# Kernel optimization log

Hardware: AMD Instinct MI355X
Metric: run time of the kernel (lower is better)

The kernel has to match this reference:

```python
import math
import jax, jax.numpy as jnp
import numpy as np

B, NQ, NK, DIM, H, HD = 2, 1024, 2048, 1024, 16, 64


def setup_inputs() -> dict:
    key = jax.random.key(0)
    ks = jax.random.split(key, 12)
    s = 1.0 / math.sqrt(DIM)
    return {
        "q": jax.random.normal(ks[0], (B, NQ, DIM), jnp.float32),
        "k": jax.random.normal(ks[1], (B, NK, DIM), jnp.float32),
        "v": jax.random.normal(ks[2], (B, NK, DIM), jnp.float32),
        "distances": jax.random.uniform(ks[3], (B, NQ, NK), jnp.float32),
        "attn_mask": jax.random.bernoulli(ks[4], 0.5, (B, NQ, NK)),
        "key_padding_mask_q": jax.random.bernoulli(ks[5], 0.5, (B, NQ)),
        "key_padding_mask_k": jax.random.bernoulli(ks[6], 0.5, (B, NK)),
        "Wq": jax.random.normal(ks[7], (H * HD, DIM), jnp.float32) * s,
        "Wk": jax.random.normal(ks[8], (H * HD, DIM), jnp.float32) * s,
        "Wv": jax.random.normal(ks[9], (H * HD, DIM), jnp.float32) * s,
        "Wo": jax.random.normal(ks[10], (DIM, H * HD), jnp.float32) * s,
        "gate_alpha": jnp.float32(0.1),
    }


def reference(q, k, v, distances, attn_mask, key_padding_mask_q,
              key_padding_mask_k, Wq, Wk, Wv, Wo, gate_alpha):
    bsz, q_len, _ = q.shape
    k_len = k.shape[1]
    neg = jnp.finfo(q.dtype).min

    # projections -> (B, H, N, HD)
    qp = (q @ Wq.T).reshape(bsz, q_len, H, HD).transpose(0, 2, 1, 3)
    kp = (k @ Wk.T).reshape(bsz, k_len, H, HD).transpose(0, 2, 1, 3)
    vp = (v @ Wv.T).reshape(bsz, k_len, H, HD).transpose(0, 2, 1, 3)

    scores = jnp.einsum('bhqd,bhkd->bhqk', qp, kp) / math.sqrt(HD)
    scores = jnp.where(attn_mask[:, None, :, :], scores, neg)
    scores = jnp.where(key_padding_mask_k[:, None, None, :], scores, neg)

    attn = jax.nn.softmax(scores, axis=-1)  # (B,H,NQ,NK)

    # distance gating: mask, batch-mean normalize, exponential gate
    d = distances * attn_mask.astype(distances.dtype)
    d = d * key_padding_mask_k[:, None, :].astype(d.dtype)
    mean = d.sum(axis=(-1, -2)) / (q_len * k_len + 1e-6)
    mean = jnp.maximum(mean, 1e-6)[:, None, None]
    d = d / mean
    alpha = jax.nn.softplus(gate_alpha)
    gate = jnp.exp(-alpha * d)[:, None, :, :]  # (B,1,NQ,NK)

    w = attn * gate
    w = w / (w.sum(axis=-1, keepdims=True) + 1e-6)

    out = jnp.einsum('bhqk,bhkd->bhqd', w, vp)
    out = out.transpose(0, 2, 1, 3).reshape(bsz, q_len, H * HD)
    out = out * key_padding_mask_q[:, :, None].astype(out.dtype)
    return out @ Wo.T
```

## Files before the change

### kernel.cpp

```cpp
#include <hip/hip_runtime.h>
#include <hip/hip_bf16.h>
#include <cfloat>

#define B_   2
#define NQ_  1024
#define NK_  2048
#define H_   16
#define HD_  64
#define VPAD 2176
#define GPAD 2112

typedef float  floatx4 __attribute__((ext_vector_type(4)));
typedef __bf16 bf16x8  __attribute__((ext_vector_type(8)));
typedef __bf16 bf16x4  __attribute__((ext_vector_type(4)));

static __device__ __forceinline__ floatx4 mfma16(bf16x8 a, bf16x8 b, floatx4 c) {
    return __builtin_amdgcn_mfma_f32_16x16x32_bf16(a, b, c, 0, 0, 0);
}

static __device__ __forceinline__ void gl_lds(const __bf16* g, __bf16* lbase,
                                              int lane) {
#if __has_builtin(__builtin_amdgcn_global_load_lds)
    __builtin_amdgcn_global_load_lds(
        (const __attribute__((address_space(1))) void*)g,
        (__attribute__((address_space(3))) void*)lbase, 16, 0, 0);
#else
    *(bf16x8*)(lbase + lane * 8) = *(const bf16x8*)g;
#endif
}

struct CvtArgs {
    const float* src[7];
    __bf16*      dst[7];
};

__global__ __launch_bounds__(256) void cvt_mean_kernel(
    CvtArgs a, const float* __restrict__ dist, const int* __restrict__ amask,
    const int* __restrict__ kpmk, float* __restrict__ msum,
    __bf16* __restrict__ dmask)
{
    if (blockIdx.x >= 1792) {
        const int mb = blockIdx.x - 1792;
        const int b  = mb >> 9;
        const float* d  = dist  + (size_t)b * NQ_ * NK_;
        const int*   am = amask + (size_t)b * NQ_ * NK_;
        const int*   km = kpmk  + b * NK_;
        __bf16*      dm = dmask + (size_t)b * NQ_ * GPAD;
        const int base = (mb & 511) * 256 + threadIdx.x;
        float s = 0.f;
        #pragma unroll
        for (int j = 0; j < 4; j++) {
            const int i   = base + j * 131072;
            const int idx = i * 4;
            const int kk  = idx & (NK_ - 1);
            const int q   = i >> 9;
            float4 dv = *(const float4*)(d + idx);
            int4   mv = *(const int4*)(am + idx);
            int4   kv = *(const int4*)(km + kk);
            bf16x4 o;
            if (mv.x && kv.x) { s += dv.x; o[0] = (__bf16)dv.x; } else o[0] = (__bf16)3e38f;
            if (mv.y && kv.y) { s += dv.y; o[1] = (__bf16)dv.y; } else o[1] = (__bf16)3e38f;
            if (mv.z && kv.z) { s += dv.z; o[2] = (__bf16)dv.z; } else o[2] = (__bf16)3e38f;
            if (mv.w && kv.w) { s += dv.w; o[3] = (__bf16)dv.w; } else o[3] = (__bf16)3e38f;
            *(bf16x4*)&dm[(size_t)q * GPAD + kk] = o;
        }
        #pragma unroll
        for (int off = 32; off >= 1; off >>= 1) s += __shfl_down(s, off);
        __shared__ float wsum[4];
        if ((threadIdx.x & 63) == 0) wsum[threadIdx.x >> 6] = s;
        __syncthreads();
        if (threadIdx.x == 0)
            atomicAdd(&msum[b], wsum[0] + wsum[1] + wsum[2] + wsum[3]);
        return;
    }
    #pragma unroll
    for (int j = 0; j < 4; j++) {
        size_t r = (size_t)blockIdx.x * 1024 + j * 256 + threadIdx.x;
        int s;
        if (r < 262144)                  { s = 0; }
        else if ((r -= 262144) < 524288) { s = 1; }
        else if ((r -= 524288) < 524288) { s = 2; }
        else { r -= 524288; s = 3 + (int)(r >> 17); r &= 131071; }
        const float* sp = a.src[s] + r * 8;
        float4 f0 = *(const float4*)sp;
        float4 f1 = *(const float4*)(sp + 4);
        bf16x8 o;
        o[0] = (__bf16)f0.x; o[1] = (__bf16)f0.y; o[2] = (__bf16)f0.z; o[3] = (__bf16)f0.w;
        o[4] = (__bf16)f1.x; o[5] = (__bf16)f1.y; o[6] = (__bf16)f1.z; o[7] = (__bf16)f1.w;
        *(bf16x8*)(a.dst[s] + r * 8) = o;
    }
}

template <typename EPI>
static __device__ __forceinline__ void gemm128_core(
    const __bf16* __restrict__ A, const __bf16* __restrict__ Bw,
    int m0, int n0, __bf16* As, __bf16* Bs, EPI epi)
{
    const int t    = threadIdx.x;
    const int w    = t >> 6, lane = t & 63;
    const int lrow = lane & 15, quad = lane >> 4;
    const int lr   = lane >> 2, lc = lane & 3;

    floatx4 acc[4][4];
    #pragma unroll
    for (int mi = 0; mi < 4; mi++)
        #pragma unroll
        for (int ni = 0; ni < 4; ni++) acc[mi][ni] = floatx4{0.f, 0.f, 0.f, 0.f};

    const __bf16* ga = A  + (size_t)(m0 + w * 32 + lr) * 1024 + lc * 8;
    const __bf16* gb = Bw + (size_t)(n0 + w * 32 + lr) * 1024 + lc * 8;

    for (int k0 = 0; k0 < 1024; k0 += 64) {
        __syncthreads();
        #pragma unroll
        for (int h = 0; h < 2; h++) {
            gl_lds(ga + k0 + h * 32,             &As[h * 4096 + (w * 32) * 32],      lane);
            gl_lds(ga + k0 + h * 32 + 16 * 1024, &As[h * 4096 + (w * 32 + 16) * 32], lane);
            gl_lds(gb + k0 + h * 32,             &Bs[h * 4096 + (w * 32) * 32],      lane);
            gl_lds(gb + k0 + h * 32 + 16 * 1024, &Bs[h * 4096 + (w * 32 + 16) * 32], lane);
        }
        __syncthreads();

        #pragma unroll
        for (int h = 0; h < 2; h++) {
            bf16x8 af[4], bfr[4];
            #pragma unroll
            for (int mi = 0; mi < 4; mi++)
                af[mi] = *(const bf16x8*)
                    &As[h * 4096 + ((w & 1) * 64 + mi * 16 + lrow) * 32 + quad * 8];
            #pragma unroll
            for (int ni = 0; ni < 4; ni++)
                bfr[ni] = *(const bf16x8*)
                    &Bs[h * 4096 + ((w >> 1) * 64 + ni * 16 + lrow) * 32 + quad * 8];
            #pragma unroll
            for (int mi = 0; mi < 4; mi++)
                #pragma unroll
                for (int ni = 0; ni < 4; ni++)
                    acc[mi][ni] = mfma16(af[mi], bfr[ni], acc[mi][ni]);
        }
    }

    #pragma unroll
    for (int mi = 0; mi < 4; mi++)
        #pragma unroll
        for (int ni = 0; ni < 4; ni++)
            #pragma unroll
            for (int r = 0; r < 4; r++) {
                const int m = m0 + (w & 1) * 64 + mi * 16 + quad * 4 + r;
                const int n = n0 + (w >> 1) * 64 + ni * 16 + lrow;
                epi(m, n, acc[mi][ni][r]);
            }
}

template <typename EPI>
static __device__ __forceinline__ void gemm32_core(
    const __bf16* __restrict__ A, const __bf16* __restrict__ Bw,
    int m0, int n0, EPI epi)
{
    __shared__ alignas(16) __bf16 As[2][32 * 32];
    __shared__ alignas(16) __bf16 Bs[2][128 * 32];
    const int t    = threadIdx.x;
    const int w    = t >> 6, lane = t & 63;
    const int lrow = lane & 15, quad = lane >> 4;
    const int lr   = lane >> 2, lc = lane & 3;

    floatx4 acc[2][2];
    #pragma unroll
    for (int mi = 0; mi < 2; mi++)
        #pragma unroll
        for (int ni = 0; ni < 2; ni++) acc[mi][ni] = floatx4{0.f, 0.f, 0.f, 0.f};

    const __bf16* ga = A  + (size_t)(m0 + (w & 1) * 16 + lr) * 1024 + lc * 8;
    const __bf16* gb = Bw + (size_t)(n0 + w * 32 + lr) * 1024 + lc * 8;

    for (int k0 = 0; k0 < 1024; k0 += 64) {
        __syncthreads();
        #pragma unroll
        for (int h = 0; h < 2; h++) {
            if (w < 2)
                gl_lds(ga + k0 + h * 32, &As[h][(w * 16) * 32], lane);
            gl_lds(gb + k0 + h * 32,             &Bs[h][(w * 32) * 32],      lane);
            gl_lds(gb + k0 + h * 32 + 16 * 1024, &Bs[h][(w * 32 + 16) * 32], lane);
        }
        __syncthreads();

        #pragma unroll
        for (int h = 0; h < 2; h++) {
            bf16x8 af[2], bfr[2];
            #pragma unroll
            for (int mi = 0; mi < 2; mi++)
                af[mi] = *(const bf16x8*)
                    &As[h][(mi * 16 + lrow) * 32 + quad * 8];
            #pragma unroll
            for (int ni = 0; ni < 2; ni++)
                bfr[ni] = *(const bf16x8*)
                    &Bs[h][(w * 32 + ni * 16 + lrow) * 32 + quad * 8];
            #pragma unroll
            for (int mi = 0; mi < 2; mi++)
                #pragma unroll
                for (int ni = 0; ni < 2; ni++)
                    acc[mi][ni] = mfma16(af[mi], bfr[ni], acc[mi][ni]);
        }
    }

    #pragma unroll
    for (int mi = 0; mi < 2; mi++)
        #pragma unroll
        for (int ni = 0; ni < 2; ni++)
            #pragma unroll
            for (int r = 0; r < 4; r++) {
                const int m = m0 + mi * 16 + quad * 4 + r;
                const int n = n0 + w * 32 + ni * 16 + lrow;
                epi(m, n, acc[mi][ni][r]);
            }
}

__global__ __launch_bounds__(256) void proj_kernel(
    const __bf16* __restrict__ qb, const __bf16* __restrict__ kb,
    const __bf16* __restrict__ vb, const __bf16* __restrict__ wqb,
    const __bf16* __restrict__ wkb, const __bf16* __restrict__ wvb,
    __bf16* __restrict__ qp, __bf16* __restrict__ kp,
    __bf16* __restrict__ vpT)
{
    __shared__ alignas(16) __bf16 As[2 * 128 * 32];
    __shared__ alignas(16) __bf16 Bs[2 * 128 * 32];
    const int z = blockIdx.z;
    if (z == 0) {
        if ((int)blockIdx.x >= 16) return;
        gemm128_core(qb, wqb, blockIdx.x * 128, blockIdx.y * 128, As, Bs,
                     [&](int m, int n, float v) {
            const int b = m >> 10, q = m & 1023;
            const int h = n >> 6,  d = n & 63;
            qp[(((size_t)(b * 16 + h) * NQ_ + q) << 6) + d] = (__bf16)v;
        });
    } else if (z == 1) {
        gemm128_core(kb, wkb, blockIdx.x * 128, blockIdx.y * 128, As, Bs,
                     [&](int m, int n, float v) {
            const int b = m >> 11, key = m & 2047;
            const int h = n >> 6,  d = n & 63;
            kp[(((size_t)(b * 16 + h) * NK_ + key) << 6) + d] = (__bf16)v;
        });
    } else {
        gemm128_core(wvb, vb, blockIdx.y * 128, blockIdx.x * 128, As, Bs,
                     [&](int m, int n, float v) {
            const int h = m >> 6,  d = m & 63;
            const int b = n >> 11, key = n & 2047;
            vpT[((size_t)(b * 16 + h) * HD_ + d) * VPAD + key] = (__bf16)v;
        });
    }
}

__global__ __launch_bounds__(256) void oproj_kernel(
    const __bf16* __restrict__ A, const __bf16* __restrict__ W,
    float* __restrict__ Cout)
{
    const int m0 = blockIdx.x * 32, n0 = blockIdx.y * 128;
    gemm32_core(A, W, m0, n0, [&](int m, int n, float v) {
        Cout[(size_t)m * 1024 + n] = v;
    });
}

__global__ __launch_bounds__(256, 2) void attn_kernel(
    const __bf16* __restrict__ qp, const __bf16* __restrict__ kp,
    const __bf16* __restrict__ vpT, const __bf16* __restrict__ dmask,
    const float* __restrict__ msum, const float* __restrict__ galpha,
    const int* __restrict__ kpmq, __bf16* __restrict__ attnout)
{
    __shared__ __bf16 Ks[64 * 72];
    __shared__ __bf16 Vt[2][64 * 72];
    __shared__ __bf16 Ps[4][2][16 * 72];
    const int t    = threadIdx.x;
    const int w    = t >> 6, lane = t & 63;
    const int lrow = lane & 15, quad = lane >> 4;
    const int qt   = blockIdx.x;
    const int bh   = blockIdx.y;
    const int b    = bh >> 4, h = bh & 15;
    const int q0   = qt * 64 + w * 16;
    const int NT   = NK_ / 64;

    const float mean  = fmaxf(msum[b] / ((float)(NQ_ * NK_) + 1e-6f), 1e-6f);
    const float alpha = log1pf(__expf(galpha[0]));
    const float cg    = -alpha / mean;

    const __bf16* qb = qp + ((size_t)bh * NQ_ + q0 + lrow) * HD_ + quad * 8;
    const bf16x8 qf0 = *(const bf16x8*)qb;
    const bf16x8 qf1 = *(const bf16x8*)(qb + 32);

    const int srow0 = t >> 3,        sc0 = t & 7;
    const int srow1 = 32 + (t >> 3), sc1 = t & 7;
    const int so0 = srow0 * 72 + sc0 * 8;
    const int so1 = srow1 * 72 + sc1 * 8;
    const __bf16* Kg = kp  + (size_t)bh * NK_ * HD_;
    const __bf16* Vg = vpT + (size_t)bh * HD_ * VPAD;
    const __bf16* grow = dmask + ((size_t)b * NQ_ + q0 + lrow) * GPAD;

    float G = 0.f;
    floatx4 O[4];
    #pragma unroll
    for (int nb = 0; nb < 4; nb++) O[nb] = floatx4{0.f, 0.f, 0.f, 0.f};

    bf16x8 kr0, kr1, vr0, vr1;
    bf16x4 gr[4];
    auto loadt = [&](int kb) {
        kr0 = *(const bf16x8*)(Kg + (size_t)(kb + srow0) * HD_ + sc0 * 8);
        kr1 = *(const bf16x8*)(Kg + (size_t)(kb + srow1) * HD_ + sc1 * 8);
        vr0 = *(const bf16x8*)(Vg + (size_t)srow0 * VPAD + kb + sc0 * 8);
        vr1 = *(const bf16x8*)(Vg + (size_t)srow1 * VPAD + kb + sc1 * 8);
        #pragma unroll
        for (int c = 0; c < 4; c++)
            gr[c] = *(const bf16x4*)(grow + kb + c * 16 + quad * 4);
    };
    loadt(0);

    for (int ib = 0; ib < NT; ib++) {
        const int kb  = ib * 64;
        const int cur = ib & 1;

        __syncthreads();
        *(bf16x8*)&Ks[so0]      = kr0;
        *(bf16x8*)&Ks[so1]      = kr1;
        *(bf16x8*)&Vt[cur][so0] = vr0;
        *(bf16x8*)&Vt[cur][so1] = vr1;
        __syncthreads();

        bf16x4 gcur[4];
        #pragma unroll
        for (int c = 0; c < 4; c++) gcur[c] = gr[c];
        if (ib + 1 < NT) loadt(kb + 64);

        floatx4 s4[4];
        #pragma unroll
        for (int c = 0; c < 4; c++) {
            bf16x8 kf0 = *(const bf16x8*)&Ks[(c * 16 + lrow) * 72 + quad * 8];
            bf16x8 kf1 = *(const bf16x8*)&Ks[(c * 16 + lrow) * 72 + 32 + quad * 8];
            floatx4 a = floatx4{0.f, 0.f, 0.f, 0.f};
            a = mfma16(kf0, qf0, a);
            a = mfma16(kf1, qf1, a);
            s4[c] = a;
        }

        if (ib > 0) {
            const int prv = cur ^ 1;
            bf16x8 pf0 = *(const bf16x8*)&Ps[w][prv][lrow * 72 + quad * 8];
            bf16x8 pf1 = *(const bf16x8*)&Ps[w][prv][lrow * 72 + 32 + quad * 8];
            #pragma unroll
            for (int nb = 0; nb < 4; nb++) {
                bf16x8 vf0 = *(const bf16x8*)
                    &Vt[prv][(nb * 16 + lrow) * 72 + quad * 8];
                bf16x8 vf1 = *(const bf16x8*)
                    &Vt[prv][(nb * 16 + lrow) * 72 + 32 + quad * 8];
                O[nb] = mfma16(pf0, vf0, O[nb]);
                O[nb] = mfma16(pf1, vf1, O[nb]);
            }
        }

        #pragma unroll
        for (int c = 0; c < 4; c++) {
            const float e0 = __expf(fmaf(s4[c][0], 0.125f, cg * (float)gcur[c][0]));
            const float e1 = __expf(fmaf(s4[c][1], 0.125f, cg * (float)gcur[c][1]));
            const float e2 = __expf(fmaf(s4[c][2], 0.125f, cg * (float)gcur[c][2]));
            const float e3 = __expf(fmaf(s4[c][3], 0.125f, cg * (float)gcur[c][3]));
            G += (e0 + e1) + (e2 + e3);
            bf16x4 pk;
            pk[0] = (__bf16)e0; pk[1] = (__bf16)e1;
            pk[2] = (__bf16)e2; pk[3] = (__bf16)e3;
            *(bf16x4*)&Ps[w][cur][lrow * 72 + c * 16 + quad * 4] = pk;
        }
    }

    {
        const int prv = (NT - 1) & 1;
        bf16x8 pf0 = *(const bf16x8*)&Ps[w][prv][lrow * 72 + quad * 8];
        bf16x8 pf1 = *(const bf16x8*)&Ps[w][prv][lrow * 72 + 32 + quad * 8];
        #pragma unroll
        for (int nb = 0; nb < 4; nb++) {
            bf16x8 vf0 = *(const bf16x8*)&Vt[prv][(nb * 16 + lrow) * 72 + quad * 8];
            bf16x8 vf1 = *(const bf16x8*)&Vt[prv][(nb * 16 + lrow) * 72 + 32 + quad * 8];
            O[nb] = mfma16(pf0, vf0, O[nb]);
            O[nb] = mfma16(pf1, vf1, O[nb]);
        }
    }

    G += __shfl_xor(G, 16);
    G += __shfl_xor(G, 32);

    #pragma unroll
    for (int r = 0; r < 4; r++) {
        const int q  = q0 + quad * 4 + r;
        const float gq = __shfl(G, quad * 4 + r);
        const float f  = kpmq[b * NQ_ + q] ? 1.f / (gq + 1e-30f) : 0.f;
        #pragma unroll
        for (int nb = 0; nb < 4; nb++) {
            attnout[((size_t)b * NQ_ + q) * 1024 + h * HD_ + nb * 16 + lrow] =
                (__bf16)(O[nb][r] * f);
        }
    }
}

extern "C" void kernel_launch(void* const* d_in, const int* in_sizes, int n_in,
                              void* d_out, int out_size, void* d_ws,
                              size_t ws_size, hipStream_t stream)
{
    const float* q      = (const float*)d_in[0];
    const float* k      = (const float*)d_in[1];
    const float* v      = (const float*)d_in[2];
    const float* dist   = (const float*)d_in[3];
    const int*   amask  = (const int*)d_in[4];
    const int*   kpmq   = (const int*)d_in[5];
    const int*   kpmk   = (const int*)d_in[6];
    const float* Wq     = (const float*)d_in[7];
    const float* Wk     = (const float*)d_in[8];
    const float* Wv     = (const float*)d_in[9];
    const float* Wo     = (const float*)d_in[10];
    const float* galpha = (const float*)d_in[11];

    char* p = (char*)d_ws;
    float*  msum = (float*)p;                 p += 256;
    __bf16* qb   = (__bf16*)p;                p += (size_t)2097152 * 2;
    __bf16* kb   = (__bf16*)p;                p += (size_t)4194304 * 2;
    __bf16* vb   = (__bf16*)p;                p += (size_t)4194304 * 2;
    __bf16* wqb  = (__bf16*)p;                p += (size_t)1048576 * 2;
    __bf16* wkb  = (__bf16*)p;                p += (size_t)1048576 * 2;
    __bf16* wvb  = (__bf16*)p;                p += (size_t)1048576 * 2;
    __bf16* wob  = (__bf16*)p;                p += (size_t)1048576 * 2;
    __bf16* qp   = (__bf16*)p;                p += (size_t)2097152 * 2;
    __bf16* kpb  = (__bf16*)p;                p += (size_t)4194304 * 2;
    __bf16* vpT  = (__bf16*)p;                p += (size_t)32 * 64 * VPAD * 2;
    __bf16* dmask = (__bf16*)p;               p += (size_t)2048 * GPAD * 2;
    __bf16* attnout = (__bf16*)p;             p += (size_t)2097152 * 2;

    CvtArgs ca;
    ca.src[0] = q;  ca.src[1] = k;  ca.src[2] = v;
    ca.src[3] = Wq; ca.src[4] = Wk; ca.src[5] = Wv; ca.src[6] = Wo;
    ca.dst[0] = qb;  ca.dst[1] = kb;  ca.dst[2] = vb;
    ca.dst[3] = wqb; ca.dst[4] = wkb; ca.dst[5] = wvb; ca.dst[6] = wob;

    hipMemsetAsync(msum, 0, 256, stream);
    cvt_mean_kernel<<<2816, 256, 0, stream>>>(ca, dist, amask, kpmk, msum,
                                              dmask);
    proj_kernel<<<dim3(32, 8, 3), 256, 0, stream>>>(qb, kb, vb, wqb, wkb, wvb,
                                                    qp, kpb, vpT);
    attn_kernel<<<dim3(16, 32), 256, 0, stream>>>(qp, kpb, vpT, dmask,
                                                  msum, galpha, kpmq, attnout);
    oproj_kernel<<<dim3(64, 8), 256, 0, stream>>>(attnout, wob, (float*)d_out);
}
```

Before: 246.5 us.

## Split attention over key dimension into two halves with combine kernel

Splits the attention kernel along the key axis into two chunks, which doubles the grid from 512 to 1024 blocks so more CUs stay busy. Each block writes unnormalized fp32 partial outputs and row sums into reused workspace buffers, and a new combine kernel adds the two halves, applies the normalization and the query padding mask, and writes bf16. Block IDs are remapped in an interleaved order, and s_setprio raises wave priority around the MFMA section. The cost is an extra launch plus a round trip of the fp32 partials through global memory.

```diff
diff --git a/kernel.cpp b/kernel.cpp
--- a/kernel.cpp
+++ b/kernel.cpp
@@ -264,7 +264,7 @@
     const __bf16* __restrict__ qp, const __bf16* __restrict__ kp,
     const __bf16* __restrict__ vpT, const __bf16* __restrict__ dmask,
     const float* __restrict__ msum, const float* __restrict__ galpha,
-    const int* __restrict__ kpmq, __bf16* __restrict__ attnout)
+    float* __restrict__ Opart, float* __restrict__ Gpart)
 {
     __shared__ __bf16 Ks[64 * 72];
     __shared__ __bf16 Vt[2][64 * 72];
@@ -272,11 +272,14 @@
     const int t    = threadIdx.x;
     const int w    = t >> 6, lane = t & 63;
     const int lrow = lane & 15, quad = lane >> 4;
-    const int qt   = blockIdx.x;
-    const int bh   = blockIdx.y;
+    const int bid  = ((blockIdx.x & 7) << 7) | (blockIdx.x >> 3);
+    const int qt   = bid & 15;
+    const int bh   = (bid >> 4) & 31;
+    const int z    = bid >> 9;
     const int b    = bh >> 4, h = bh & 15;
     const int q0   = qt * 64 + w * 16;
-    const int NT   = NK_ / 64;
+    const int kb0  = z * (NK_ / 2);
+    const int NT   = NK_ / 128;
 
     const float mean  = fmaxf(msum[b] / ((float)(NQ_ * NK_) + 1e-6f), 1e-6f);
     const float alpha = log1pf(__expf(galpha[0]));
@@ -290,9 +293,9 @@
     const int srow1 = 32 + (t >> 3), sc1 = t & 7;
     const int so0 = srow0 * 72 + sc0 * 8;
     const int so1 = srow1 * 72 + sc1 * 8;
-    const __bf16* Kg = kp  + (size_t)bh * NK_ * HD_;
-    const __bf16* Vg = vpT + (size_t)bh * HD_ * VPAD;
-    const __bf16* grow = dmask + ((size_t)b * NQ_ + q0 + lrow) * GPAD;
+    const __bf16* Kg = kp  + ((size_t)bh * NK_ + kb0) * HD_;
+    const __bf16* Vg = vpT + (size_t)bh * HD_ * VPAD + kb0;
+    const __bf16* grow = dmask + ((size_t)b * NQ_ + q0 + lrow) * GPAD + kb0;
 
     float G = 0.f;
     floatx4 O[4];
@@ -328,6 +331,7 @@
         for (int c = 0; c < 4; c++) gcur[c] = gr[c];
         if (ib + 1 < NT) loadt(kb + 64);
 
+        __builtin_amdgcn_s_setprio(1);
         floatx4 s4[4];
         #pragma unroll
         for (int c = 0; c < 4; c++) {
@@ -353,6 +357,7 @@
                 O[nb] = mfma16(pf1, vf1, O[nb]);
             }
         }
+        __builtin_amdgcn_s_setprio(0);
 
         #pragma unroll
         for (int c = 0; c < 4; c++) {
@@ -384,17 +389,40 @@
     G += __shfl_xor(G, 16);
     G += __shfl_xor(G, 32);
 
+    float* Op = Opart + (size_t)z * (B_ * NQ_ * 1024)
+                      + ((size_t)b * NQ_ + q0) * 1024 + h * HD_;
     #pragma unroll
     for (int r = 0; r < 4; r++) {
-        const int q  = q0 + quad * 4 + r;
-        const float gq = __shfl(G, quad * 4 + r);
-        const float f  = kpmq[b * NQ_ + q] ? 1.f / (gq + 1e-30f) : 0.f;
-        #pragma unroll
-        for (int nb = 0; nb < 4; nb++) {
-            attnout[((size_t)b * NQ_ + q) * 1024 + h * HD_ + nb * 16 + lrow] =
-                (__bf16)(O[nb][r] * f);
-        }
-    }
+        const int qr = quad * 4 + r;
+        #pragma unroll
+        for (int nb = 0; nb < 4; nb++)
+            Op[(size_t)qr * 1024 + nb * 16 + lrow] = O[nb][r];
+    }
+    if (lane < 16)
+        Gpart[(size_t)z * (32 * 1024) + bh * 1024 + q0 + lane] = G;
+}
+
+__global__ __launch_bounds__(256) void combine_kernel(
+    const float* __restrict__ Opart, const float* __restrict__ Gpart,
+    const int* __restrict__ kpmq, __bf16* __restrict__ attnout)
+{
+    const int idx = blockIdx.x * 256 + threadIdx.x;
+    const int m   = idx >> 8;
+    const int c4  = (idx & 255) * 4;
+    const int b   = m >> 10, q = m & 1023;
+    const int h   = c4 >> 6;
+    const float g = Gpart[(b * 16 + h) * 1024 + q]
+                  + Gpart[32 * 1024 + (b * 16 + h) * 1024 + q];
+    const float f = kpmq[b * NQ_ + q] ? 1.f / (g + 1e-30f) : 0.f;
+    const float4 o0 = *(const float4*)(Opart + (size_t)m * 1024 + c4);
+    const float4 o1 = *(const float4*)(Opart + (size_t)(B_ * NQ_) * 1024
+                                              + (size_t)m * 1024 + c4);
+    bf16x4 r;
+    r[0] = (__bf16)((o0.x + o1.x) * f);
+    r[1] = (__bf16)((o0.y + o1.y) * f);
+    r[2] = (__bf16)((o0.z + o1.z) * f);
+    r[3] = (__bf16)((o0.w + o1.w) * f);
+    *(bf16x4*)&attnout[(size_t)m * 1024 + c4] = r;
 }
 
 extern "C" void kernel_launch(void* const* d_in, const int* in_sizes, int n_in,
@@ -429,6 +457,9 @@
     __bf16* dmask = (__bf16*)p;               p += (size_t)2048 * GPAD * 2;
     __bf16* attnout = (__bf16*)p;             p += (size_t)2097152 * 2;
 
+    float* Opart = (float*)kb;
+    float* Gpart = (float*)qb;
+
     CvtArgs ca;
     ca.src[0] = q;  ca.src[1] = k;  ca.src[2] = v;
     ca.src[3] = Wq; ca.src[4] = Wk; ca.src[5] = Wv; ca.src[6] = Wo;
@@ -440,7 +471,8 @@
                                               dmask);
     proj_kernel<<<dim3(32, 8, 3), 256, 0, stream>>>(qb, kb, vb, wqb, wkb, wvb,
                                                     qp, kpb, vpT);
-    attn_kernel<<<dim3(16, 32), 256, 0, stream>>>(qp, kpb, vpT, dmask,
-                                                  msum, galpha, kpmq, attnout);
+    attn_kernel<<<1024, 256, 0, stream>>>(qp, kpb, vpT, dmask,
+                                          msum, galpha, Opart, Gpart);
+    combine_kernel<<<2048, 256, 0, stream>>>(Opart, Gpart, kpmq, attnout);
     oproj_kernel<<<dim3(64, 8), 256, 0, stream>>>(attnout, wob, (float*)d_out);
 }
```

After: 249.6 us. About the same (+1.2%).
